# Kernel optimization log

Measured on AMD Instinct MI355X. Metric: run time of the kernel, lower is better.

Reference implementation:

```python
import jax, jax.numpy as jnp
import numpy as np

K = 3      # deformable kernel size
PAD = 1    # padding for all 3x3 convs


def conv2d(x, w, b):
    y = jax.lax.conv_general_dilated(x, w, (1, 1), ((PAD, PAD), (PAD, PAD)),
                                     dimension_numbers=('NCHW', 'OIHW', 'NCHW'))
    return y + b[None, :, None, None]


def ln_channels(x, w, b, eps=1e-5):
    # Restormer 'WithBias' LayerNorm: normalize over channel dim of NCHW
    mu = jnp.mean(x, axis=1, keepdims=True)
    var = jnp.mean((x - mu) ** 2, axis=1, keepdims=True)
    return (x - mu) / jnp.sqrt(var + eps) * w[None, :, None, None] + b[None, :, None, None]


def deform_conv(x, offset, mask, weight, bias):
    # x: [B,Cin,H,W], offset: [B,2*K*K,H,W] (dy,dx interleaved), mask: [B,K*K,H,W]
    B, Cin, H, W = x.shape
    Kk = K * K
    off = offset.reshape(B, Kk, 2, H, W)
    dy, dx = off[:, :, 0], off[:, :, 1]                     # [B,Kk,H,W]
    ky, kx = jnp.meshgrid(jnp.arange(K), jnp.arange(K), indexing='ij')
    ky = (ky.reshape(-1) - PAD).astype(x.dtype)             # [Kk]
    kx = (kx.reshape(-1) - PAD).astype(x.dtype)
    py = jnp.arange(H, dtype=x.dtype)[None, None, :, None] + ky[None, :, None, None] + dy
    px = jnp.arange(W, dtype=x.dtype)[None, None, None, :] + kx[None, :, None, None] + dx
    y0 = jnp.floor(py); x0 = jnp.floor(px)
    wy1 = py - y0; wx1 = px - x0
    xf = x.reshape(B, Cin, H * W)

    def corner(yc, xc, wgt):
        valid = (yc >= 0) & (yc <= H - 1) & (xc >= 0) & (xc <= W - 1)
        yi = jnp.clip(yc, 0, H - 1).astype(jnp.int32)
        xi = jnp.clip(xc, 0, W - 1).astype(jnp.int32)
        idx = (yi * W + xi).reshape(B, -1)                  # [B, Kk*H*W]
        v = jax.vmap(lambda xb, ib: xb[:, ib])(xf, idx)     # [B, Cin, Kk*H*W]
        v = v.reshape(B, Cin, Kk, H, W)
        return v * (wgt * valid.astype(x.dtype))[:, None]

    sampled = (corner(y0, x0, (1 - wy1) * (1 - wx1))
               + corner(y0, x0 + 1, (1 - wy1) * wx1)
               + corner(y0 + 1, x0, wy1 * (1 - wx1))
               + corner(y0 + 1, x0 + 1, wy1 * wx1))         # [B,Cin,Kk,H,W]
    sampled = sampled * mask[:, None]                        # modulated (DCNv2)
    wk = weight.reshape(weight.shape[0], Cin, Kk)            # [Cout,Cin,Kk]
    out = jnp.einsum('bckhw,ock->bohw', sampled, wk)
    return out + bias[None, :, None, None]


def setup_inputs() -> dict:
    key = jax.random.key(0)
    ks = jax.random.split(key, 12)
    B, Ce, Cf, H, W = 4, 32, 64, 128, 128
    Cin, Kk = Ce + Cf, K * K
    d = {
        'f_evt_rec': jax.random.normal(ks[0], (B, Ce, H, W), jnp.float32),
        'f_efnet':   jax.random.normal(ks[1], (B, Cf, H, W), jnp.float32),
        'ln_evt_w': jnp.ones((Ce,), jnp.float32), 'ln_evt_b': jnp.zeros((Ce,), jnp.float32),
        'ln_ef_w':  jnp.ones((Cf,), jnp.float32), 'ln_ef_b':  jnp.zeros((Cf,), jnp.float32),
        'ln_al_w':  jnp.ones((Cf,), jnp.float32), 'ln_al_b':  jnp.zeros((Cf,), jnp.float32),
        'off_w': jax.random.normal(ks[2], (2 * Kk, Cin, K, K), jnp.float32) * 0.01,
        'off_b': jnp.zeros((2 * Kk,), jnp.float32),
        'mod_w': jax.random.normal(ks[3], (Kk, Cin, K, K), jnp.float32) * 0.01,
        'mod_b': jnp.zeros((Kk,), jnp.float32),
        'reg_w': jax.random.normal(ks[4], (Cf, Cin, K, K), jnp.float32) * 0.05,
        'reg_b': jnp.zeros((Cf,), jnp.float32),
        'stage_idx': 0,
    }
    return d


def reference(f_evt_rec, f_efnet, ln_evt_w, ln_evt_b, ln_ef_w, ln_ef_b,
              ln_al_w, ln_al_b, off_w, off_b, mod_w, mod_b, reg_w, reg_b, stage_idx):
    e = ln_channels(f_evt_rec, ln_evt_w, ln_evt_b)
    fe = ln_channels(f_efnet, ln_ef_w, ln_ef_b)
    ox = jnp.concatenate([e, fe], axis=1)                    # [B,96,H,W]
    offset = conv2d(ox, off_w, off_b)
    mask = 2.0 * jax.nn.sigmoid(conv2d(ox, mod_w, mod_b))
    al = deform_conv(ox, offset, mask, reg_w, reg_b)         # [B,64,H,W]
    al = jnp.where(al >= 0, al, 0.2 * al)                    # LeakyReLU(0.2)
    al = ln_channels(al, ln_al_w, ln_al_b)
    return al
```

## Files before the change

### kernel.cpp

```cpp
#include <hip/hip_runtime.h>
#include <hip/hip_bf16.h>

#define BATCH 4
#define HH 128
#define WW 128
#define CE 32
#define CF 64
#define CIN 96
#define KK 9
#define COUT 64

typedef __bf16 bf16x8 __attribute__((ext_vector_type(8)));
typedef float f32x4 __attribute__((ext_vector_type(4)));
#define MFMA16(a, b, c) __builtin_amdgcn_mfma_f32_16x16x32_bf16(a, b, c, 0, 0, 0)
typedef union { uint4 u; bf16x8 v; } U8;

#define OX_BYTES   (BATCH * HH * WW * CIN * 2)
#define WCT_OFFB   OX_BYTES
#define WCT_BYTES  (32 * 864 * 2)
#define WKT_OFFB   (WCT_OFFB + WCT_BYTES)

__global__ void prep_weights(const float* __restrict__ off_w,
                             const float* __restrict__ mod_w,
                             const float* __restrict__ reg_w,
                             __hip_bfloat16* __restrict__ wcombT,
                             __hip_bfloat16* __restrict__ wkT) {
  int e = blockIdx.x * 256 + threadIdx.x;
  const int TOT1 = 32 * 864;
  const int TOT2 = 64 * 864;
  if (e < TOT1) {
    int oc = e / 864, k = e % 864;
    int tap = k / 96, c = k % 96;
    float v = 0.f;
    if (oc < 18)      v = off_w[(oc * CIN + c) * KK + tap];
    else if (oc < 27) v = mod_w[((oc - 18) * CIN + c) * KK + tap];
    wcombT[e] = __float2bfloat16(v);
  } else if (e < TOT1 + TOT2) {
    int e2 = e - TOT1;
    int oc = e2 / 864, k = e2 % 864;
    int tap = k / 96, c = k % 96;
    wkT[e2] = __float2bfloat16(reg_w[(oc * CIN + c) * KK + tap]);
  }
}

__global__ __launch_bounds__(256) void ln_concat(
    const float* __restrict__ evt, const float* __restrict__ efn,
    const float* __restrict__ w_e, const float* __restrict__ b_e,
    const float* __restrict__ w_f, const float* __restrict__ b_f,
    __hip_bfloat16* __restrict__ ox) {
  __shared__ float vals[64 * 97];
  __shared__ float part[4 * 64 * 4];
  __shared__ float stat[64 * 4];

  int bid = blockIdx.x;
  int wg = (bid & 7) * 128 + (bid >> 3);
  int p0 = wg * 64;
  int b = p0 >> 14, y = (p0 >> 7) & 127, x0 = p0 & 127;
  int t = threadIdx.x, px = t & 63, g = t >> 6;

  float sE = 0.f, sE2 = 0.f, sF = 0.f, sF2 = 0.f;
  const float* pe = evt + (((size_t)b * CE) << 14) + (y << 7) + x0 + px;
#pragma unroll
  for (int j = 0; j < 8; ++j) {
    int c = g * 8 + j;
    float v = pe[(size_t)c << 14];
    vals[px * 97 + c] = v; sE += v; sE2 += v * v;
  }
  const float* pf = efn + (((size_t)b * CF) << 14) + (y << 7) + x0 + px;
#pragma unroll
  for (int j = 0; j < 16; ++j) {
    int c = g * 16 + j;
    float v = pf[(size_t)c << 14];
    vals[px * 97 + CE + c] = v; sF += v; sF2 += v * v;
  }
  {
    float4 p4 = {sE, sE2, sF, sF2};
    *(float4*)&part[(g * 64 + px) * 4] = p4;
  }
  __syncthreads();
  if (g == 0) {
    float aE = 0.f, aE2 = 0.f, aF = 0.f, aF2 = 0.f;
#pragma unroll
    for (int gg = 0; gg < 4; ++gg) {
      float4 p4 = *(const float4*)&part[(gg * 64 + px) * 4];
      aE += p4.x; aE2 += p4.y; aF += p4.z; aF2 += p4.w;
    }
    float muE = aE * (1.f / CE);
    float vE = aE2 * (1.f / CE) - muE * muE;
    float muF = aF * (1.f / CF);
    float vF = aF2 * (1.f / CF) - muF * muF;
    float4 s4 = {muE, rsqrtf(vE + 1e-5f), muF, rsqrtf(vF + 1e-5f)};
    *(float4*)&stat[px * 4] = s4;
  }
  __syncthreads();
  uint* orow = (uint*)(ox + (size_t)p0 * CIN);
#pragma unroll
  for (int i = 0; i < 12; ++i) {
    int e = i * 256 + t;
    int xx = e / 48, c = (e % 48) * 2;
    float v0 = vals[xx * 97 + c], v1 = vals[xx * 97 + c + 1];
    float mu, rs, lw0, lb0, lw1, lb1;
    if (c < CE) {
      mu = stat[xx * 4 + 0]; rs = stat[xx * 4 + 1];
      lw0 = w_e[c]; lb0 = b_e[c]; lw1 = w_e[c + 1]; lb1 = b_e[c + 1];
    } else {
      mu = stat[xx * 4 + 2]; rs = stat[xx * 4 + 3];
      lw0 = w_f[c - CE]; lb0 = b_f[c - CE]; lw1 = w_f[c + 1 - CE]; lb1 = b_f[c + 1 - CE];
    }
    float o0 = (v0 - mu) * rs * lw0 + lb0;
    float o1 = (v1 - mu) * rs * lw1 + lb1;
    __hip_bfloat16 h0 = __float2bfloat16(o0), h1 = __float2bfloat16(o1);
    orow[e] = ((uint)*(unsigned short*)&h1 << 16) | (uint)*(unsigned short*)&h0;
  }
}

__device__ __forceinline__ uint blend1(uint u0, uint u1, uint u2, uint u3,
                                       float w0, float w1, float w2, float w3) {
  float lo = w0 * __uint_as_float(u0 << 16) + w1 * __uint_as_float(u1 << 16)
           + w2 * __uint_as_float(u2 << 16) + w3 * __uint_as_float(u3 << 16);
  float hi = w0 * __uint_as_float(u0 & 0xffff0000u) + w1 * __uint_as_float(u1 & 0xffff0000u)
           + w2 * __uint_as_float(u2 & 0xffff0000u) + w3 * __uint_as_float(u3 & 0xffff0000u);
  __hip_bfloat16 bl = __float2bfloat16(lo), bh = __float2bfloat16(hi);
  return ((uint)*(unsigned short*)&bh << 16) | (uint)*(unsigned short*)&bl;
}

__global__ __launch_bounds__(256) void conv_deform_fused(
    const __hip_bfloat16* __restrict__ ox,
    const __hip_bfloat16* __restrict__ wcombT,
    const __hip_bfloat16* __restrict__ wkT,
    const float* __restrict__ off_b, const float* __restrict__ mod_b,
    const float* __restrict__ reg_b,
    const float* __restrict__ lnw, const float* __restrict__ lnb,
    float* __restrict__ out) {
  __shared__ char smem[41216];
  short* At   = (short*)smem;
  float* offm = (float*)smem;
  short* SaA  = (short*)(smem + 7168);
  short* SaB  = (short*)(smem + 20480);
  float* outl = (float*)(smem + 7168);

  int bid = blockIdx.x;
  int wg = (bid & 7) * 128 + (bid >> 3);
  int p0 = wg * 64;
  int b = p0 >> 14, y = (p0 >> 7) & 127, x0 = p0 & 127;
  const __hip_bfloat16* oxb = ox + (((size_t)b) << 14) * CIN;

  int t = threadIdx.x, lane = t & 63, wv = t >> 6;
  int mw = wv >> 1, nw = wv & 1;
  int lr = lane & 15, lg = lane >> 4;

  for (int u = t; u < 3 * 66 * 12; u += 256) {
    int c8 = u % 12, pw_ = u / 12, w = pw_ % 66, r = pw_ / 66;
    int yy = y + r - 1, xx = x0 + w - 1;
    uint4 v = {0u, 0u, 0u, 0u};
    if ((unsigned)yy < 128u && (unsigned)xx < 128u)
      v = *(const uint4*)(oxb + (size_t)((yy << 7) + xx) * CIN + c8 * 8);
    *(uint4*)&At[(r * 66 + w) * 104 + c8 * 8] = v;
  }
  __syncthreads();

  f32x4 cc0 = {0.f,0.f,0.f,0.f}, cc1 = {0.f,0.f,0.f,0.f};
  {
    const __hip_bfloat16* brow = wcombT + (size_t)(nw * 16 + lr) * 864;
#pragma unroll
    for (int tap = 0; tap < 9; ++tap) {
      int dy = tap / 3, dx = tap % 3;
#pragma unroll
      for (int ks = 0; ks < 3; ++ks) {
        int ko = ks * 32 + lg * 8;
        bf16x8 a0 = *(const bf16x8*)&At[(dy * 66 + mw * 32 + lr + dx) * 104 + ko];
        bf16x8 a1 = *(const bf16x8*)&At[(dy * 66 + mw * 32 + 16 + lr + dx) * 104 + ko];
        U8 bf; bf.u = *(const uint4*)(brow + tap * 96 + ko);
        cc0 = MFMA16(a0, bf.v, cc0);
        cc1 = MFMA16(a1, bf.v, cc1);
      }
    }
  }
  __syncthreads();

  {
    int oc = nw * 16 + lr;
    if (oc < 27) {
      float bia = (oc < 18) ? off_b[oc] : mod_b[oc - 18];
#pragma unroll
      for (int mi = 0; mi < 2; ++mi) {
        f32x4 a = mi ? cc1 : cc0;
#pragma unroll
        for (int r = 0; r < 4; ++r) {
          int px2 = mw * 32 + mi * 16 + lg * 4 + r;
          float v = a[r] + bia;
          if (oc >= 18) v = 2.f / (1.f + __expf(-v));
          offm[px2 * 28 + oc] = v;
        }
      }
    }
  }
  __syncthreads();

  int px = t & 63;
  int c8b = wv * 3;
  const __hip_bfloat16* gb = oxb + c8b * 8;
  const __hip_bfloat16* wb0 = wkT + (size_t)(nw * 32 + lr) * 864;
  const __hip_bfloat16* wb1 = wkT + (size_t)(nw * 32 + 16 + lr) * 864;
  f32x4 a00 = {0.f,0.f,0.f,0.f}, a01 = {0.f,0.f,0.f,0.f};
  f32x4 a10 = {0.f,0.f,0.f,0.f}, a11 = {0.f,0.f,0.f,0.f};

  uint4 qa0,qa1,qa2,qa3, qb0,qb1,qb2,qb3, qc0,qc1,qc2,qc3;
  float pw0, pw1, pw2, pw3;

#define ISSUE(TAP)                                                           \
  {                                                                          \
    const float* om = offm + px * 28;                                        \
    float dyv = om[2 * (TAP)], dxv = om[2 * (TAP) + 1], mk = om[18 + (TAP)]; \
    float psy = (float)(y + (TAP) / 3 - 1) + dyv;                            \
    float psx = (float)(x0 + px + (TAP) % 3 - 1) + dxv;                      \
    float fy = floorf(psy), fx = floorf(psx);                                \
    float wy1 = psy - fy, wx1 = psx - fx;                                    \
    float wy0 = 1.f - wy1, wx0 = 1.f - wx1;                                  \
    int iy0 = (int)fy, ix0 = (int)fx, iy1 = iy0 + 1, ix1 = ix0 + 1;          \
    float vy0 = ((unsigned)iy0 < 128u) ? 1.f : 0.f;                          \
    float vy1 = ((unsigned)iy1 < 128u) ? 1.f : 0.f;                          \
    float vx0 = ((unsigned)ix0 < 128u) ? 1.f : 0.f;                          \
    float vx1 = ((unsigned)ix1 < 128u) ? 1.f : 0.f;                          \
    int cy0 = min(max(iy0, 0), 127), cy1 = min(max(iy1, 0), 127);            \
    int cx0 = min(max(ix0, 0), 127), cx1 = min(max(ix1, 0), 127);            \
    int i00 = ((cy0 << 7) + cx0) * CIN, i01 = ((cy0 << 7) + cx1) * CIN;      \
    int i10 = ((cy1 << 7) + cx0) * CIN, i11 = ((cy1 << 7) + cx1) * CIN;      \
    pw0 = wy0 * wx0 * vy0 * vx0 * mk; pw1 = wy0 * wx1 * vy0 * vx1 * mk;      \
    pw2 = wy1 * wx0 * vy1 * vx0 * mk; pw3 = wy1 * wx1 * vy1 * vx1 * mk;      \
    qa0 = *(const uint4*)(gb + i00);      qa1 = *(const uint4*)(gb + i01);   \
    qa2 = *(const uint4*)(gb + i10);      qa3 = *(const uint4*)(gb + i11);   \
    qb0 = *(const uint4*)(gb + i00 + 8);  qb1 = *(const uint4*)(gb + i01 + 8); \
    qb2 = *(const uint4*)(gb + i10 + 8);  qb3 = *(const uint4*)(gb + i11 + 8); \
    qc0 = *(const uint4*)(gb + i00 + 16); qc1 = *(const uint4*)(gb + i01 + 16);\
    qc2 = *(const uint4*)(gb + i10 + 16); qc3 = *(const uint4*)(gb + i11 + 16);\
  }

#define BLEND(Q0, Q1, Q2, Q3, DST)                                           \
  { uint4 rv;                                                                \
    rv.x = blend1(Q0.x, Q1.x, Q2.x, Q3.x, pw0, pw1, pw2, pw3);               \
    rv.y = blend1(Q0.y, Q1.y, Q2.y, Q3.y, pw0, pw1, pw2, pw3);               \
    rv.z = blend1(Q0.z, Q1.z, Q2.z, Q3.z, pw0, pw1, pw2, pw3);               \
    rv.w = blend1(Q0.w, Q1.w, Q2.w, Q3.w, pw0, pw1, pw2, pw3);               \
    *(uint4*)&(DST) = rv; }

  ISSUE(0);
  int buf = 0;
  for (int tap = 0; tap < 9; ++tap) {
    short* S = buf ? SaB : SaA;
    BLEND(qa0, qa1, qa2, qa3, S[px * 104 + (c8b + 0) * 8]);
    BLEND(qb0, qb1, qb2, qb3, S[px * 104 + (c8b + 1) * 8]);
    BLEND(qc0, qc1, qc2, qc3, S[px * 104 + (c8b + 2) * 8]);
    if (tap < 8) ISSUE(tap + 1);
    __syncthreads();
#pragma unroll
    for (int ks = 0; ks < 3; ++ks) {
      int ko = ks * 32 + lg * 8;
      bf16x8 fa0 = *(const bf16x8*)&S[(mw * 32 + lr) * 104 + ko];
      bf16x8 fa1 = *(const bf16x8*)&S[(mw * 32 + 16 + lr) * 104 + ko];
      U8 b0, b1;
      b0.u = *(const uint4*)(wb0 + tap * 96 + ko);
      b1.u = *(const uint4*)(wb1 + tap * 96 + ko);
      a00 = MFMA16(fa0, b0.v, a00);
      a01 = MFMA16(fa0, b1.v, a01);
      a10 = MFMA16(fa1, b0.v, a10);
      a11 = MFMA16(fa1, b1.v, a11);
    }
    buf ^= 1;
  }
  __syncthreads();

#pragma unroll
  for (int mi = 0; mi < 2; ++mi)
#pragma unroll
  for (int ni = 0; ni < 2; ++ni) {
    int oc = nw * 32 + ni * 16 + lr;
    float bia = reg_b[oc];
    f32x4 a = (mi == 0) ? (ni == 0 ? a00 : a01) : (ni == 0 ? a10 : a11);
#pragma unroll
    for (int r = 0; r < 4; ++r) {
      int px2 = mw * 32 + mi * 16 + lg * 4 + r;
      float v = a[r] + bia;
      v = (v >= 0.f) ? v : 0.2f * v;
      outl[px2 * 68 + oc] = v;
    }
  }
  __syncthreads();
  {
    int px2 = t >> 2, part = t & 3;
    float s = 0.f, s2 = 0.f;
#pragma unroll
    for (int j = 0; j < 16; ++j) {
      float v = outl[px2 * 68 + part * 16 + j];
      s += v; s2 += v * v;
    }
    s += __shfl_xor(s, 1); s2 += __shfl_xor(s2, 1);
    s += __shfl_xor(s, 2); s2 += __shfl_xor(s2, 2);
    float mu = s * (1.f / 64.f);
    float var = s2 * (1.f / 64.f) - mu * mu;
    float rs = rsqrtf(var + 1e-5f);
    size_t ob = (size_t)b * COUT * 16384 + (size_t)y * 128 + x0 + px2;
#pragma unroll
    for (int j = 0; j < 16; ++j) {
      int oc = part * 16 + j;
      float v = outl[px2 * 68 + oc];
      out[ob + (size_t)oc * 16384] = (v - mu) * rs * lnw[oc] + lnb[oc];
    }
  }
#undef ISSUE
#undef BLEND
}

extern "C" void kernel_launch(void* const* d_in, const int* in_sizes, int n_in,
                              void* d_out, int out_size, void* d_ws, size_t ws_size,
                              hipStream_t stream) {
  const float* evt      = (const float*)d_in[0];
  const float* efn      = (const float*)d_in[1];
  const float* ln_evt_w = (const float*)d_in[2];
  const float* ln_evt_b = (const float*)d_in[3];
  const float* ln_ef_w  = (const float*)d_in[4];
  const float* ln_ef_b  = (const float*)d_in[5];
  const float* ln_al_w  = (const float*)d_in[6];
  const float* ln_al_b  = (const float*)d_in[7];
  const float* off_w    = (const float*)d_in[8];
  const float* off_b    = (const float*)d_in[9];
  const float* mod_w    = (const float*)d_in[10];
  const float* mod_b    = (const float*)d_in[11];
  const float* reg_w    = (const float*)d_in[12];
  const float* reg_b    = (const float*)d_in[13];
  float* out = (float*)d_out;

  char* wsb = (char*)d_ws;
  __hip_bfloat16* oxb    = (__hip_bfloat16*)wsb;
  __hip_bfloat16* wcombT = (__hip_bfloat16*)(wsb + WCT_OFFB);
  __hip_bfloat16* wkT    = (__hip_bfloat16*)(wsb + WKT_OFFB);

  prep_weights<<<(32 * 864 + 64 * 864 + 255) / 256, 256, 0, stream>>>(
      off_w, mod_w, reg_w, wcombT, wkT);
  ln_concat<<<BATCH * HH * WW / 64, 256, 0, stream>>>(
      evt, efn, ln_evt_w, ln_evt_b, ln_ef_w, ln_ef_b, oxb);
  conv_deform_fused<<<BATCH * HH * WW / 64, 256, 0, stream>>>(
      oxb, wcombT, wkT, off_b, mod_b, reg_b, ln_al_w, ln_al_b, out);
}
```

Measured before the change: 174.6 us.

## Restructure deform kernel to per-wave pixel tiles without shared staging or barriers

Folds the weight-prep kernel into the LayerNorm/concat kernel, saving one launch. Reworks the fused conv/deform kernel so each wave owns 16 pixels across all output channels. The wave reads conv inputs straight from global memory instead of a shared halo tile, and feeds bilinear-blended samples to MFMA from registers instead of double-buffered shared memory. This drops every __syncthreads, shrinks LDS and sets launch bounds to 4 blocks per CU for occupancy, at the cost of redundant global loads, more weight reads per wave and more register pressure.

```diff
diff --git a/kernel.cpp b/kernel.cpp
--- a/kernel.cpp
+++ b/kernel.cpp
@@ -20,37 +20,36 @@
 #define WCT_BYTES  (32 * 864 * 2)
 #define WKT_OFFB   (WCT_OFFB + WCT_BYTES)
 
-__global__ void prep_weights(const float* __restrict__ off_w,
-                             const float* __restrict__ mod_w,
-                             const float* __restrict__ reg_w,
-                             __hip_bfloat16* __restrict__ wcombT,
-                             __hip_bfloat16* __restrict__ wkT) {
-  int e = blockIdx.x * 256 + threadIdx.x;
-  const int TOT1 = 32 * 864;
-  const int TOT2 = 64 * 864;
-  if (e < TOT1) {
-    int oc = e / 864, k = e % 864;
-    int tap = k / 96, c = k % 96;
-    float v = 0.f;
-    if (oc < 18)      v = off_w[(oc * CIN + c) * KK + tap];
-    else if (oc < 27) v = mod_w[((oc - 18) * CIN + c) * KK + tap];
-    wcombT[e] = __float2bfloat16(v);
-  } else if (e < TOT1 + TOT2) {
-    int e2 = e - TOT1;
-    int oc = e2 / 864, k = e2 % 864;
-    int tap = k / 96, c = k % 96;
-    wkT[e2] = __float2bfloat16(reg_w[(oc * CIN + c) * KK + tap]);
-  }
-}
-
-__global__ __launch_bounds__(256) void ln_concat(
+__global__ __launch_bounds__(256) void ln_concat_prep(
     const float* __restrict__ evt, const float* __restrict__ efn,
     const float* __restrict__ w_e, const float* __restrict__ b_e,
     const float* __restrict__ w_f, const float* __restrict__ b_f,
-    __hip_bfloat16* __restrict__ ox) {
+    const float* __restrict__ off_w, const float* __restrict__ mod_w,
+    const float* __restrict__ reg_w,
+    __hip_bfloat16* __restrict__ ox,
+    __hip_bfloat16* __restrict__ wcombT,
+    __hip_bfloat16* __restrict__ wkT) {
   __shared__ float vals[64 * 97];
   __shared__ float part[4 * 64 * 4];
   __shared__ float stat[64 * 4];
+
+  {
+    int e = blockIdx.x * 256 + threadIdx.x;
+    const int TOT1 = 32 * 864, TOT2 = 64 * 864;
+    if (e < TOT1) {
+      int oc = e / 864, k = e % 864;
+      int tap = k / 96, c = k % 96;
+      float v = 0.f;
+      if (oc < 18)      v = off_w[(oc * CIN + c) * KK + tap];
+      else if (oc < 27) v = mod_w[((oc - 18) * CIN + c) * KK + tap];
+      wcombT[e] = __float2bfloat16(v);
+    } else if (e < TOT1 + TOT2) {
+      int e2 = e - TOT1;
+      int oc = e2 / 864, k = e2 % 864;
+      int tap = k / 96, c = k % 96;
+      wkT[e2] = __float2bfloat16(reg_w[(oc * CIN + c) * KK + tap]);
+    }
+  }
 
   int bid = blockIdx.x;
   int wg = (bid & 7) * 128 + (bid >> 3);
@@ -124,7 +123,7 @@
   return ((uint)*(unsigned short*)&bh << 16) | (uint)*(unsigned short*)&bl;
 }
 
-__global__ __launch_bounds__(256) void conv_deform_fused(
+__global__ __launch_bounds__(256, 4) void conv_deform_fused(
     const __hip_bfloat16* __restrict__ ox,
     const __hip_bfloat16* __restrict__ wcombT,
     const __hip_bfloat16* __restrict__ wkT,
@@ -132,12 +131,8 @@
     const float* __restrict__ reg_b,
     const float* __restrict__ lnw, const float* __restrict__ lnb,
     float* __restrict__ out) {
-  __shared__ char smem[41216];
-  short* At   = (short*)smem;
-  float* offm = (float*)smem;
-  short* SaA  = (short*)(smem + 7168);
-  short* SaB  = (short*)(smem + 20480);
-  float* outl = (float*)(smem + 7168);
+  __shared__ float offm[64 * 28];
+  __shared__ float outl[64 * 65];
 
   int bid = blockIdx.x;
   int wg = (bid & 7) * 128 + (bid >> 3);
@@ -146,74 +141,60 @@
   const __hip_bfloat16* oxb = ox + (((size_t)b) << 14) * CIN;
 
   int t = threadIdx.x, lane = t & 63, wv = t >> 6;
-  int mw = wv >> 1, nw = wv & 1;
   int lr = lane & 15, lg = lane >> 4;
-
-  for (int u = t; u < 3 * 66 * 12; u += 256) {
-    int c8 = u % 12, pw_ = u / 12, w = pw_ % 66, r = pw_ / 66;
-    int yy = y + r - 1, xx = x0 + w - 1;
-    uint4 v = {0u, 0u, 0u, 0u};
-    if ((unsigned)yy < 128u && (unsigned)xx < 128u)
-      v = *(const uint4*)(oxb + (size_t)((yy << 7) + xx) * CIN + c8 * 8);
-    *(uint4*)&At[(r * 66 + w) * 104 + c8 * 8] = v;
-  }
-  __syncthreads();
+  int pxw = (wv << 4) + lr;
 
   f32x4 cc0 = {0.f,0.f,0.f,0.f}, cc1 = {0.f,0.f,0.f,0.f};
   {
-    const __hip_bfloat16* brow = wcombT + (size_t)(nw * 16 + lr) * 864;
-#pragma unroll
+    const __hip_bfloat16* br0 = wcombT + (size_t)lr * 864 + lg * 8;
+    const __hip_bfloat16* br1 = wcombT + (size_t)(16 + lr) * 864 + lg * 8;
     for (int tap = 0; tap < 9; ++tap) {
-      int dy = tap / 3, dx = tap % 3;
+      int yy = y + tap / 3 - 1;
+      int xx = x0 + pxw + tap % 3 - 1;
+      bool valid = ((unsigned)yy < 128u) && ((unsigned)xx < 128u);
+      int cy = min(max(yy, 0), 127), cx = min(max(xx, 0), 127);
+      const __hip_bfloat16* arow = oxb + (size_t)((cy << 7) + cx) * CIN + lg * 8;
 #pragma unroll
       for (int ks = 0; ks < 3; ++ks) {
-        int ko = ks * 32 + lg * 8;
-        bf16x8 a0 = *(const bf16x8*)&At[(dy * 66 + mw * 32 + lr + dx) * 104 + ko];
-        bf16x8 a1 = *(const bf16x8*)&At[(dy * 66 + mw * 32 + 16 + lr + dx) * 104 + ko];
-        U8 bf; bf.u = *(const uint4*)(brow + tap * 96 + ko);
-        cc0 = MFMA16(a0, bf.v, cc0);
-        cc1 = MFMA16(a1, bf.v, cc1);
+        U8 a, w0, w1;
+        a.u = *(const uint4*)(arow + ks * 32);
+        if (!valid) { a.u.x = 0; a.u.y = 0; a.u.z = 0; a.u.w = 0; }
+        w0.u = *(const uint4*)(br0 + tap * 96 + ks * 32);
+        w1.u = *(const uint4*)(br1 + tap * 96 + ks * 32);
+        cc0 = MFMA16(a.v, w0.v, cc0);
+        cc1 = MFMA16(a.v, w1.v, cc1);
       }
     }
   }
-  __syncthreads();
-
-  {
-    int oc = nw * 16 + lr;
+#pragma unroll
+  for (int nt = 0; nt < 2; ++nt) {
+    int oc = nt * 16 + lr;
     if (oc < 27) {
       float bia = (oc < 18) ? off_b[oc] : mod_b[oc - 18];
-#pragma unroll
-      for (int mi = 0; mi < 2; ++mi) {
-        f32x4 a = mi ? cc1 : cc0;
-#pragma unroll
-        for (int r = 0; r < 4; ++r) {
-          int px2 = mw * 32 + mi * 16 + lg * 4 + r;
-          float v = a[r] + bia;
-          if (oc >= 18) v = 2.f / (1.f + __expf(-v));
-          offm[px2 * 28 + oc] = v;
-        }
+      f32x4 a = nt ? cc1 : cc0;
+#pragma unroll
+      for (int r = 0; r < 4; ++r) {
+        int pxc = (wv << 4) + (lg << 2) + r;
+        float v = a[r] + bia;
+        if (oc >= 18) v = 2.f / (1.f + __expf(-v));
+        offm[pxc * 28 + oc] = v;
       }
     }
   }
-  __syncthreads();
-
-  int px = t & 63;
-  int c8b = wv * 3;
-  const __hip_bfloat16* gb = oxb + c8b * 8;
-  const __hip_bfloat16* wb0 = wkT + (size_t)(nw * 32 + lr) * 864;
-  const __hip_bfloat16* wb1 = wkT + (size_t)(nw * 32 + 16 + lr) * 864;
-  f32x4 a00 = {0.f,0.f,0.f,0.f}, a01 = {0.f,0.f,0.f,0.f};
-  f32x4 a10 = {0.f,0.f,0.f,0.f}, a11 = {0.f,0.f,0.f,0.f};
+
+  const float* om = offm + pxw * 28;
+  const __hip_bfloat16* gb = oxb + lg * 8;
+  f32x4 ac0 = {0.f,0.f,0.f,0.f}, ac1 = {0.f,0.f,0.f,0.f};
+  f32x4 ac2 = {0.f,0.f,0.f,0.f}, ac3 = {0.f,0.f,0.f,0.f};
 
   uint4 qa0,qa1,qa2,qa3, qb0,qb1,qb2,qb3, qc0,qc1,qc2,qc3;
   float pw0, pw1, pw2, pw3;
 
-#define ISSUE(TAP)                                                           \
+#define ISSUE(T)                                                             \
   {                                                                          \
-    const float* om = offm + px * 28;                                        \
-    float dyv = om[2 * (TAP)], dxv = om[2 * (TAP) + 1], mk = om[18 + (TAP)]; \
-    float psy = (float)(y + (TAP) / 3 - 1) + dyv;                            \
-    float psx = (float)(x0 + px + (TAP) % 3 - 1) + dxv;                      \
+    float dyv = om[2 * (T)], dxv = om[2 * (T) + 1], mk = om[18 + (T)];       \
+    float psy = (float)(y + (T) / 3 - 1) + dyv;                              \
+    float psx = (float)(x0 + pxw + (T) % 3 - 1) + dxv;                       \
     float fy = floorf(psy), fx = floorf(psx);                                \
     float wy1 = psy - fy, wx1 = psx - fx;                                    \
     float wy0 = 1.f - wy1, wx0 = 1.f - wx1;                                  \
@@ -230,68 +211,68 @@
     pw2 = wy1 * wx0 * vy1 * vx0 * mk; pw3 = wy1 * wx1 * vy1 * vx1 * mk;      \
     qa0 = *(const uint4*)(gb + i00);      qa1 = *(const uint4*)(gb + i01);   \
     qa2 = *(const uint4*)(gb + i10);      qa3 = *(const uint4*)(gb + i11);   \
-    qb0 = *(const uint4*)(gb + i00 + 8);  qb1 = *(const uint4*)(gb + i01 + 8); \
-    qb2 = *(const uint4*)(gb + i10 + 8);  qb3 = *(const uint4*)(gb + i11 + 8); \
-    qc0 = *(const uint4*)(gb + i00 + 16); qc1 = *(const uint4*)(gb + i01 + 16);\
-    qc2 = *(const uint4*)(gb + i10 + 16); qc3 = *(const uint4*)(gb + i11 + 16);\
-  }
-
-#define BLEND(Q0, Q1, Q2, Q3, DST)                                           \
-  { uint4 rv;                                                                \
-    rv.x = blend1(Q0.x, Q1.x, Q2.x, Q3.x, pw0, pw1, pw2, pw3);               \
-    rv.y = blend1(Q0.y, Q1.y, Q2.y, Q3.y, pw0, pw1, pw2, pw3);               \
-    rv.z = blend1(Q0.z, Q1.z, Q2.z, Q3.z, pw0, pw1, pw2, pw3);               \
-    rv.w = blend1(Q0.w, Q1.w, Q2.w, Q3.w, pw0, pw1, pw2, pw3);               \
-    *(uint4*)&(DST) = rv; }
+    qb0 = *(const uint4*)(gb + i00 + 32); qb1 = *(const uint4*)(gb + i01 + 32);\
+    qb2 = *(const uint4*)(gb + i10 + 32); qb3 = *(const uint4*)(gb + i11 + 32);\
+    qc0 = *(const uint4*)(gb + i00 + 64); qc1 = *(const uint4*)(gb + i01 + 64);\
+    qc2 = *(const uint4*)(gb + i10 + 64); qc3 = *(const uint4*)(gb + i11 + 64);\
+  }
 
   ISSUE(0);
-  int buf = 0;
   for (int tap = 0; tap < 9; ++tap) {
-    short* S = buf ? SaB : SaA;
-    BLEND(qa0, qa1, qa2, qa3, S[px * 104 + (c8b + 0) * 8]);
-    BLEND(qb0, qb1, qb2, qb3, S[px * 104 + (c8b + 1) * 8]);
-    BLEND(qc0, qc1, qc2, qc3, S[px * 104 + (c8b + 2) * 8]);
-    if (tap < 8) ISSUE(tap + 1);
-    __syncthreads();
-#pragma unroll
-    for (int ks = 0; ks < 3; ++ks) {
-      int ko = ks * 32 + lg * 8;
-      bf16x8 fa0 = *(const bf16x8*)&S[(mw * 32 + lr) * 104 + ko];
-      bf16x8 fa1 = *(const bf16x8*)&S[(mw * 32 + 16 + lr) * 104 + ko];
-      U8 b0, b1;
-      b0.u = *(const uint4*)(wb0 + tap * 96 + ko);
-      b1.u = *(const uint4*)(wb1 + tap * 96 + ko);
-      a00 = MFMA16(fa0, b0.v, a00);
-      a01 = MFMA16(fa0, b1.v, a01);
-      a10 = MFMA16(fa1, b0.v, a10);
-      a11 = MFMA16(fa1, b1.v, a11);
-    }
-    buf ^= 1;
-  }
-  __syncthreads();
-
-#pragma unroll
-  for (int mi = 0; mi < 2; ++mi)
-#pragma unroll
-  for (int ni = 0; ni < 2; ++ni) {
-    int oc = nw * 32 + ni * 16 + lr;
+    U8 fa0, fa1, fa2;
+    fa0.u.x = blend1(qa0.x, qa1.x, qa2.x, qa3.x, pw0, pw1, pw2, pw3);
+    fa0.u.y = blend1(qa0.y, qa1.y, qa2.y, qa3.y, pw0, pw1, pw2, pw3);
+    fa0.u.z = blend1(qa0.z, qa1.z, qa2.z, qa3.z, pw0, pw1, pw2, pw3);
+    fa0.u.w = blend1(qa0.w, qa1.w, qa2.w, qa3.w, pw0, pw1, pw2, pw3);
+    fa1.u.x = blend1(qb0.x, qb1.x, qb2.x, qb3.x, pw0, pw1, pw2, pw3);
+    fa1.u.y = blend1(qb0.y, qb1.y, qb2.y, qb3.y, pw0, pw1, pw2, pw3);
+    fa1.u.z = blend1(qb0.z, qb1.z, qb2.z, qb3.z, pw0, pw1, pw2, pw3);
+    fa1.u.w = blend1(qb0.w, qb1.w, qb2.w, qb3.w, pw0, pw1, pw2, pw3);
+    fa2.u.x = blend1(qc0.x, qc1.x, qc2.x, qc3.x, pw0, pw1, pw2, pw3);
+    fa2.u.y = blend1(qc0.y, qc1.y, qc2.y, qc3.y, pw0, pw1, pw2, pw3);
+    fa2.u.z = blend1(qc0.z, qc1.z, qc2.z, qc3.z, pw0, pw1, pw2, pw3);
+    fa2.u.w = blend1(qc0.w, qc1.w, qc2.w, qc3.w, pw0, pw1, pw2, pw3);
+    if (tap < 8) {
+      int tn = tap + 1;
+      ISSUE(tn);
+    }
+    const __hip_bfloat16* wr = wkT + (size_t)lr * 864 + tap * 96 + lg * 8;
+    U8 b0, b1, b2;
+#define MSTEP(ACC, ROWOFF)                                                   \
+    b0.u = *(const uint4*)(wr + (ROWOFF) * 864);                             \
+    b1.u = *(const uint4*)(wr + (ROWOFF) * 864 + 32);                        \
+    b2.u = *(const uint4*)(wr + (ROWOFF) * 864 + 64);                        \
+    ACC = MFMA16(fa0.v, b0.v, ACC);                                          \
+    ACC = MFMA16(fa1.v, b1.v, ACC);                                          \
+    ACC = MFMA16(fa2.v, b2.v, ACC);
+    MSTEP(ac0, 0)
+    MSTEP(ac1, 16)
+    MSTEP(ac2, 32)
+    MSTEP(ac3, 48)
+#undef MSTEP
+  }
+#undef ISSUE
+
+#pragma unroll
+  for (int nt = 0; nt < 4; ++nt) {
+    int oc = nt * 16 + lr;
     float bia = reg_b[oc];
-    f32x4 a = (mi == 0) ? (ni == 0 ? a00 : a01) : (ni == 0 ? a10 : a11);
+    f32x4 a = (nt == 0) ? ac0 : (nt == 1) ? ac1 : (nt == 2) ? ac2 : ac3;
 #pragma unroll
     for (int r = 0; r < 4; ++r) {
-      int px2 = mw * 32 + mi * 16 + lg * 4 + r;
+      int pxc = (wv << 4) + (lg << 2) + r;
       float v = a[r] + bia;
       v = (v >= 0.f) ? v : 0.2f * v;
-      outl[px2 * 68 + oc] = v;
-    }
-  }
-  __syncthreads();
+      outl[pxc * 65 + oc] = v;
+    }
+  }
   {
-    int px2 = t >> 2, part = t & 3;
+    int px2 = (wv << 4) + (lane >> 2);
+    int part = lane & 3;
     float s = 0.f, s2 = 0.f;
 #pragma unroll
     for (int j = 0; j < 16; ++j) {
-      float v = outl[px2 * 68 + part * 16 + j];
+      float v = outl[px2 * 65 + part * 16 + j];
       s += v; s2 += v * v;
     }
     s += __shfl_xor(s, 1); s2 += __shfl_xor(s2, 1);
@@ -303,12 +284,10 @@
 #pragma unroll
     for (int j = 0; j < 16; ++j) {
       int oc = part * 16 + j;
-      float v = outl[px2 * 68 + oc];
+      float v = outl[px2 * 65 + oc];
       out[ob + (size_t)oc * 16384] = (v - mu) * rs * lnw[oc] + lnb[oc];
     }
   }
-#undef ISSUE
-#undef BLEND
 }
 
 extern "C" void kernel_launch(void* const* d_in, const int* in_sizes, int n_in,
@@ -335,10 +314,9 @@
   __hip_bfloat16* wcombT = (__hip_bfloat16*)(wsb + WCT_OFFB);
   __hip_bfloat16* wkT    = (__hip_bfloat16*)(wsb + WKT_OFFB);
 
-  prep_weights<<<(32 * 864 + 64 * 864 + 255) / 256, 256, 0, stream>>>(
-      off_w, mod_w, reg_w, wcombT, wkT);
-  ln_concat<<<BATCH * HH * WW / 64, 256, 0, stream>>>(
-      evt, efn, ln_evt_w, ln_evt_b, ln_ef_w, ln_ef_b, oxb);
+  ln_concat_prep<<<BATCH * HH * WW / 64, 256, 0, stream>>>(
+      evt, efn, ln_evt_w, ln_evt_b, ln_ef_w, ln_ef_b,
+      off_w, mod_w, reg_w, oxb, wcombT, wkT);
   conv_deform_fused<<<BATCH * HH * WW / 64, 256, 0, stream>>>(
       oxb, wcombT, wkT, off_b, mod_b, reg_b, ln_al_w, ln_al_b, out);
 }
```

After: 188.7 us. 8.1% more time.
